# Kernel optimization log

Hardware: AMD Instinct MI355X
Metric: run time of the kernel (lower is better)

## Reference

```python
import jax, jax.numpy as jnp
import numpy as np

N, E, B = 30000, 480000, 64
F_IN, HID, ED = 128, 64, 32
NEG, EPS = 0.2, 1e-5


def _add_self_loops(edge_index, edge_attr):
    # PyG add_self_loops with fill_value='mean': self-loop edge_attr of node i
    # is the mean of edge_attr over edges whose destination is i.
    src, dst = edge_index[0], edge_index[1]
    cnt = jax.ops.segment_sum(jnp.ones((edge_attr.shape[0],), edge_attr.dtype), dst, num_segments=N)
    mean = jax.ops.segment_sum(edge_attr, dst, num_segments=N) / jnp.maximum(cnt, 1.0)[:, None]
    loop = jnp.arange(N)
    return jnp.concatenate([src, loop]), jnp.concatenate([dst, loop]), jnp.concatenate([edge_attr, mean], axis=0)


def _gat_conv(x, src, dst, ea, W, We, a_s, a_d, a_e, bias, H, Fo):
    xs = (x @ W).reshape(-1, H, Fo)              # [N, H, Fo]
    al_src = (xs * a_s).sum(-1)                  # [N, H]
    al_dst = (xs * a_d).sum(-1)                  # [N, H]
    ef = (ea @ We).reshape(-1, H, Fo)            # [Et, H, Fo]
    alpha = al_src[src] + al_dst[dst] + (ef * a_e).sum(-1)   # [Et, H]
    alpha = jax.nn.leaky_relu(alpha, NEG)
    # softmax over incoming edges of each destination node (segment softmax)
    m = jax.ops.segment_max(alpha, dst, num_segments=N)
    ex = jnp.exp(alpha - m[dst])
    s = jax.ops.segment_sum(ex, dst, num_segments=N)
    w = ex / s[dst]                              # [Et, H]
    out = jax.ops.segment_sum(xs[src] * w[:, :, None], dst, num_segments=N)
    return out.reshape(-1, H * Fo) + bias


def _bn(x, g, b):
    # BatchNorm1d in training mode: biased batch statistics over nodes
    mu = x.mean(0)
    var = x.var(0)
    return (x - mu) * jax.lax.rsqrt(var + EPS) * g + b


def _pool(x, batch, Wg, bg):
    # GlobalAttention: softmax(gate_nn(x)) per graph, weighted sum of x
    gate = (x @ Wg + bg)[:, 0]                   # [N]
    m = jax.ops.segment_max(gate, batch, num_segments=B)
    e = jnp.exp(gate - m[batch])
    s = jax.ops.segment_sum(e, batch, num_segments=B)
    w = e / s[batch]
    return jax.ops.segment_sum(x * w[:, None], batch, num_segments=B)   # [B, HID]


def setup_inputs():
    k = jax.random.split(jax.random.key(0), 16)
    g = lambda i, shape, fan: jax.random.normal(k[i], shape, jnp.float32) / np.sqrt(fan)
    return {
        "x": jax.random.normal(k[0], (N, F_IN), jnp.float32),
        "edge_attr": jax.random.normal(k[1], (E, ED), jnp.float32),
        "edge_index": jax.random.randint(k[2], (2, E), 0, N),
        "batch": jnp.sort(jax.random.randint(k[3], (N,), 0, B)),
        "W1": g(4, (F_IN, 4 * HID), F_IN),
        "We1": g(5, (ED, 4 * HID), ED),
        "att_src1": g(6, (4, HID), HID),
        "att_dst1": g(7, (4, HID), HID),
        "att_edge1": g(8, (4, HID), HID),
        "bias1": jnp.zeros((4 * HID,), jnp.float32),
        "g1": jnp.ones((4 * HID,), jnp.float32),
        "b1": jnp.zeros((4 * HID,), jnp.float32),
        "W2": g(9, (4 * HID, HID), 4 * HID),
        "We2": g(10, (ED, HID), ED),
        "att_src2": g(11, (1, HID), HID),
        "att_dst2": g(12, (1, HID), HID),
        "att_edge2": g(13, (1, HID), HID),
        "bias2": jnp.zeros((HID,), jnp.float32),
        "g2": jnp.ones((HID,), jnp.float32),
        "b2": jnp.zeros((HID,), jnp.float32),
        "Wg": g(14, (HID, 1), HID),
        "bg": jnp.zeros((1,), jnp.float32),
    }


def reference(x, edge_attr, edge_index, batch, W1, We1, att_src1, att_dst1, att_edge1, bias1, g1, b1, W2, We2, att_src2, att_dst2, att_edge2, bias2, g2, b2, Wg, bg):
    src, dst, ea = _add_self_loops(edge_index, edge_attr)
    h = jax.nn.relu(_bn(_gat_conv(x, src, dst, ea, W1, We1, att_src1, att_dst1, att_edge1, bias1, 4, HID), g1, b1))
    h = jax.nn.relu(_bn(_gat_conv(h, src, dst, ea, W2, We2, att_src2, att_dst2, att_edge2, bias2, 1, HID), g2, b2))
    return _pool(h, batch, Wg, bg)
```

## Files before the change

### kernel.cpp

```cpp
#include <hip/hip_runtime.h>
#include <math.h>

#define NN 30000
#define EE 480000
#define BB 64

typedef __bf16 b16x8 __attribute__((ext_vector_type(8)));
typedef float  f32x4 __attribute__((ext_vector_type(4)));
typedef unsigned short u16x8 __attribute__((ext_vector_type(8)));

__device__ __forceinline__ float wsum64(float v){
  #pragma unroll
  for (int m = 32; m >= 1; m >>= 1) v += __shfl_xor(v, m, 64);
  return v;
}
__device__ __forceinline__ float wmax64(float v){
  #pragma unroll
  for (int m = 32; m >= 1; m >>= 1) v = fmaxf(v, __shfl_xor(v, m, 64));
  return v;
}
__device__ __forceinline__ float wsum16(float v){
  #pragma unroll
  for (int m = 1; m < 16; m <<= 1) v += __shfl_xor(v, m, 64);
  return v;
}
__device__ __forceinline__ unsigned short f2b(float f){
  union { float f; unsigned u; } v; v.f = f;
  unsigned r = v.u + 0x7fffu + ((v.u >> 16) & 1u);
  return (unsigned short)(r >> 16);
}
__device__ __forceinline__ float b2f(unsigned short u){
  union { unsigned u; float f; } v; v.u = ((unsigned)u) << 16;
  return v.f;
}

__global__ void hist_kernel(const int* __restrict__ dst, int* __restrict__ deg){
  int e = blockIdx.x*256 + threadIdx.x;
  if (e < EE) atomicAdd(&deg[dst[e]], 1);
}

__global__ __launch_bounds__(256) void scan_kernel(const int* __restrict__ deg, int* __restrict__ rowptr){
  __shared__ int s[256];
  __shared__ int wred[4];
  const int b = blockIdx.x, tid = threadIdx.x;
  const int base = b*256;
  int part = 0;
  for (int idx = tid; idx < base; idx += 256) part += deg[idx];
  #pragma unroll
  for (int m = 32; m >= 1; m >>= 1) part += __shfl_xor(part, m, 64);
  if ((tid & 63) == 0) wred[tid >> 6] = part;
  __syncthreads();
  int offset = wred[0] + wred[1] + wred[2] + wred[3];
  int n = base + tid;
  int d = (n < NN) ? deg[n] : 0;
  s[tid] = d;
  __syncthreads();
  for (int off = 1; off < 256; off <<= 1){
    int v = (tid >= off) ? s[tid - off] : 0;
    __syncthreads();
    s[tid] += v;
    __syncthreads();
  }
  if (n < NN) rowptr[n] = offset + s[tid] - d;
  if (b == 0 && tid == 0) rowptr[NN] = EE;
}

__global__ void prep_kernel(const float* __restrict__ W1, const float* __restrict__ W2,
                            const float* __restrict__ We1, const float* __restrict__ ae1,
                            const float* __restrict__ We2, const float* __restrict__ ae2,
                            unsigned short* __restrict__ W1t, unsigned short* __restrict__ W2t,
                            float* __restrict__ wae){
  int t = threadIdx.x, b = blockIdx.x;
  if (b < 128){
    W1t[t*128 + b] = f2b(W1[b*256 + t]);
  } else if (b < 384){
    int k = b - 128;
    if (t < 64) W2t[t*256 + k] = f2b(W2[k*64 + t]);
  } else {
    if (t < 128){
      int h = t >> 5, k = t & 31;
      float s = 0.f;
      for (int f = 0; f < 64; f++) s += We1[k*256 + h*64 + f] * ae1[h*64 + f];
      wae[h*32 + k] = s;
    } else if (t < 160){
      int k = t - 128;
      float s = 0.f;
      for (int f = 0; f < 64; f++) s += We2[k*64 + f] * ae2[f];
      wae[128 + k] = s;
    }
  }
}

__global__ __launch_bounds__(256) void edot_scatter_kernel(const float* __restrict__ ea,
    const float* __restrict__ wae, const int* __restrict__ src, const int* __restrict__ dst,
    const int* __restrict__ rowptr, int* __restrict__ cursor, float* __restrict__ rec){
  __shared__ float s_w[160];
  if (threadIdx.x < 160) s_w[threadIdx.x] = wae[threadIdx.x];
  __syncthreads();
  const int lane = threadIdx.x & 63;
  const int il = lane & 7;
  const int e = blockIdx.x*32 + (threadIdx.x >> 3);
  if (e >= EE) return;
  float4 v = *(const float4*)(ea + (size_t)e*32 + il*4);
  float dots[5];
  #pragma unroll
  for (int h = 0; h < 5; h++){
    float4 w = *(const float4*)&s_w[h*32 + il*4];
    dots[h] = v.x*w.x + v.y*w.y + v.z*w.z + v.w*w.w;
  }
  #pragma unroll
  for (int m = 1; m < 8; m <<= 1)
    #pragma unroll
    for (int h = 0; h < 5; h++) dots[h] += __shfl_xor(dots[h], m, 64);
  int slot = 0;
  if (il == 0){
    int dd = dst[e];
    slot = rowptr[dd] + atomicAdd(&cursor[dd], 1);
  }
  slot = __shfl(slot, lane & ~7, 64);
  if (il == 0){
    float4 lo; lo.x = dots[0]; lo.y = dots[1]; lo.z = dots[2]; lo.w = dots[3];
    *(float4*)(rec + (size_t)slot*8) = lo;
  } else if (il == 1){
    float4 hi; hi.x = dots[4]; hi.y = __int_as_float(src[e]); hi.z = 0.f; hi.w = 0.f;
    *(float4*)(rec + (size_t)slot*8 + 4) = hi;
  }
}

__global__ __launch_bounds__(256) void gemm1_mfma(const float* __restrict__ x,
    const unsigned short* __restrict__ Bt, const float* __restrict__ a_s, const float* __restrict__ a_d,
    unsigned short* __restrict__ out, float* __restrict__ alsrc, float* __restrict__ aldst){
  __shared__ unsigned short As[128*136];
  __shared__ unsigned short Bs[64*136];
  const int tid = threadIdx.x;
  const int w = tid >> 6, lane = tid & 63;
  const int c = lane & 15, gq = lane >> 4;
  const int m0 = blockIdx.x * 128;
  #pragma unroll
  for (int q = 0; q < 16; q++){
    int ch = tid*16 + q;
    int r = ch >> 5, off = (ch & 31)*4;
    int grow = m0 + r;
    ushort4 o;
    if (grow < NN){
      float4 v = *(const float4*)(x + (size_t)grow*128 + off);
      o.x = f2b(v.x); o.y = f2b(v.y); o.z = f2b(v.z); o.w = f2b(v.w);
    } else o = make_ushort4(0,0,0,0);
    *(ushort4*)&As[r*136 + off] = o;
  }
  #pragma unroll
  for (int q = 0; q < 4; q++){
    int ch = tid*4 + q;
    int n = ch >> 4, off = (ch & 15)*8;
    *(ulonglong2*)&Bs[n*136 + off] = *(const ulonglong2*)(Bt + (size_t)n*128 + off);
  }
  __syncthreads();
  for (int head = 0; head < 4; head++){
    f32x4 acc[2][4];
    #pragma unroll
    for (int mt = 0; mt < 2; mt++)
      #pragma unroll
      for (int nt = 0; nt < 4; nt++) acc[mt][nt] = (f32x4){0.f,0.f,0.f,0.f};
    #pragma unroll
    for (int k0 = 0; k0 < 128; k0 += 32){
      b16x8 afr[2], bfr[4];
      #pragma unroll
      for (int mt = 0; mt < 2; mt++)
        afr[mt] = *(const b16x8*)&As[(w*32 + mt*16 + c)*136 + k0 + gq*8];
      #pragma unroll
      for (int nt = 0; nt < 4; nt++)
        bfr[nt] = *(const b16x8*)&Bs[(nt*16 + c)*136 + k0 + gq*8];
      #pragma unroll
      for (int mt = 0; mt < 2; mt++)
        #pragma unroll
        for (int nt = 0; nt < 4; nt++)
          acc[mt][nt] = __builtin_amdgcn_mfma_f32_16x16x32_bf16(afr[mt], bfr[nt], acc[mt][nt], 0, 0, 0);
    }
    __syncthreads();
    if (head < 3){
      #pragma unroll
      for (int q = 0; q < 4; q++){
        int ch = tid*4 + q;
        int n = ch >> 4, off = (ch & 15)*8;
        *(ulonglong2*)&Bs[n*136 + off] = *(const ulonglong2*)(Bt + (size_t)((head+1)*64 + n)*128 + off);
      }
    }
    float asv[4], adv[4];
    #pragma unroll
    for (int nt = 0; nt < 4; nt++){
      asv[nt] = a_s[head*64 + nt*16 + c];
      adv[nt] = a_d[head*64 + nt*16 + c];
    }
    #pragma unroll
    for (int mt = 0; mt < 2; mt++){
      int base_row = m0 + w*32 + mt*16 + gq*4;
      #pragma unroll
      for (int r = 0; r < 4; r++){
        int row = base_row + r;
        float ps = 0.f, pd = 0.f;
        #pragma unroll
        for (int nt = 0; nt < 4; nt++){
          ps += acc[mt][nt][r] * asv[nt];
          pd += acc[mt][nt][r] * adv[nt];
        }
        ps = wsum16(ps); pd = wsum16(pd);
        if (row < NN){
          if (c == 0){
            alsrc[(size_t)row*4 + head] = ps;
            aldst[(size_t)row*4 + head] = pd;
          }
          #pragma unroll
          for (int nt = 0; nt < 4; nt++)
            out[(size_t)row*256 + head*64 + nt*16 + c] = f2b(acc[mt][nt][r]);
        }
      }
    }
    if (head < 3) __syncthreads();
  }
}

__global__ __launch_bounds__(256) void gemm2_mfma(const unsigned short* __restrict__ Ab,
    const unsigned short* __restrict__ Bt,
    const float* __restrict__ cs, const float* __restrict__ csq,
    const float* __restrict__ g, const float* __restrict__ b,
    const float* __restrict__ a_s, const float* __restrict__ a_d,
    unsigned short* __restrict__ out, float* __restrict__ alsrc, float* __restrict__ aldst){
  __shared__ unsigned short As[128*136];
  __shared__ unsigned short Bs[64*136];
  __shared__ float s_scale[256], s_shift[256];
  const int tid = threadIdx.x;
  const int w = tid >> 6, lane = tid & 63;
  const int c = lane & 15, gq = lane >> 4;
  const int m0 = blockIdx.x * 128;
  if (tid < 256){
    float mu  = cs[tid]  * (1.f/NN);
    float var = csq[tid] * (1.f/NN) - mu*mu;
    float rs  = rsqrtf(var + 1e-5f);
    float sc  = rs * g[tid];
    s_scale[tid] = sc;
    s_shift[tid] = b[tid] - mu*sc;
  }
  __syncthreads();
  f32x4 acc[2][4];
  #pragma unroll
  for (int mt = 0; mt < 2; mt++)
    #pragma unroll
    for (int nt = 0; nt < 4; nt++) acc[mt][nt] = (f32x4){0.f,0.f,0.f,0.f};
  for (int kp = 0; kp < 256; kp += 128){
    #pragma unroll
    for (int q = 0; q < 16; q++){
      int ch = tid*16 + q;
      int r = ch >> 5, off = (ch & 31)*4;
      int grow = m0 + r;
      ushort4 o;
      if (grow < NN){
        ushort4 v = *(const ushort4*)(Ab + (size_t)grow*256 + kp + off);
        float4 sc = *(const float4*)&s_scale[kp + off];
        float4 sh = *(const float4*)&s_shift[kp + off];
        o.x = f2b(fmaxf(fmaf(b2f(v.x), sc.x, sh.x), 0.f));
        o.y = f2b(fmaxf(fmaf(b2f(v.y), sc.y, sh.y), 0.f));
        o.z = f2b(fmaxf(fmaf(b2f(v.z), sc.z, sh.z), 0.f));
        o.w = f2b(fmaxf(fmaf(b2f(v.w), sc.w, sh.w), 0.f));
      } else o = make_ushort4(0,0,0,0);
      *(ushort4*)&As[r*136 + off] = o;
    }
    #pragma unroll
    for (int q = 0; q < 4; q++){
      int ch = tid*4 + q;
      int n = ch >> 4, off = (ch & 15)*8;
      *(ulonglong2*)&Bs[n*136 + off] = *(const ulonglong2*)(Bt + (size_t)n*256 + kp + off);
    }
    __syncthreads();
    #pragma unroll
    for (int k0 = 0; k0 < 128; k0 += 32){
      b16x8 afr[2], bfr[4];
      #pragma unroll
      for (int mt = 0; mt < 2; mt++)
        afr[mt] = *(const b16x8*)&As[(w*32 + mt*16 + c)*136 + k0 + gq*8];
      #pragma unroll
      for (int nt = 0; nt < 4; nt++)
        bfr[nt] = *(const b16x8*)&Bs[(nt*16 + c)*136 + k0 + gq*8];
      #pragma unroll
      for (int mt = 0; mt < 2; mt++)
        #pragma unroll
        for (int nt = 0; nt < 4; nt++)
          acc[mt][nt] = __builtin_amdgcn_mfma_f32_16x16x32_bf16(afr[mt], bfr[nt], acc[mt][nt], 0, 0, 0);
    }
    __syncthreads();
  }
  float asv[4], adv[4];
  #pragma unroll
  for (int nt = 0; nt < 4; nt++){
    asv[nt] = a_s[nt*16 + c];
    adv[nt] = a_d[nt*16 + c];
  }
  #pragma unroll
  for (int mt = 0; mt < 2; mt++){
    int base_row = m0 + w*32 + mt*16 + gq*4;
    #pragma unroll
    for (int r = 0; r < 4; r++){
      int row = base_row + r;
      float ps = 0.f, pd = 0.f;
      #pragma unroll
      for (int nt = 0; nt < 4; nt++){
        ps += acc[mt][nt][r] * asv[nt];
        pd += acc[mt][nt][r] * adv[nt];
      }
      ps = wsum16(ps); pd = wsum16(pd);
      if (row < NN){
        if (c == 0){
          alsrc[row] = ps;
          aldst[row] = pd;
        }
        #pragma unroll
        for (int nt = 0; nt < 4; nt++)
          out[(size_t)row*64 + nt*16 + c] = f2b(acc[mt][nt][r]);
      }
    }
  }
}

template<int H>
__global__ __launch_bounds__(256) void agg_kernel(const int* __restrict__ rowptr,
    const float* __restrict__ rec,
    const float* __restrict__ al_src, const float* __restrict__ al_dst,
    const unsigned short* __restrict__ xsb, const float* __restrict__ bias,
    unsigned short* __restrict__ outb, float* __restrict__ outf){
  constexpr int CH = 128;
  __shared__ float s_e_all[4][CH*H];
  __shared__ int   s_src_all[4][CH];
  const int wid  = threadIdx.x >> 6;
  const int lane = threadIdx.x & 63;
  const int i = blockIdx.x*4 + wid;
  float* s_e  = s_e_all[wid];
  int*   s_src = s_src_all[wid];
  const int r0 = rowptr[i];
  const int d  = rowptr[i+1] - r0;
  float ad[H], asi[H];
  #pragma unroll
  for (int h = 0; h < H; h++){ ad[h] = al_dst[(size_t)i*H+h]; asi[h] = al_src[(size_t)i*H+h]; }
  float sesum[H], m[H];
  #pragma unroll
  for (int h = 0; h < H; h++){ sesum[h] = 0.f; m[h] = -1e30f; }
  for (int t = lane; t < d; t += 64){
    const float* rp = rec + (size_t)(r0 + t)*8;
    float al[H];
    int sn;
    if constexpr (H == 4){
      float4 ev = *(const float4*)rp;
      float2 hi = *(const float2*)(rp + 4);
      sn = __float_as_int(hi.y);
      float4 av = *(const float4*)(al_src + (size_t)sn*4);
      al[0]=av.x+ad[0]+ev.x; al[1]=av.y+ad[1]+ev.y; al[2]=av.z+ad[2]+ev.z; al[3]=av.w+ad[3]+ev.w;
      sesum[0]+=ev.x; sesum[1]+=ev.y; sesum[2]+=ev.z; sesum[3]+=ev.w;
    } else {
      float2 hi = *(const float2*)(rp + 4);
      sn = __float_as_int(hi.y);
      al[0] = al_src[sn] + ad[0] + hi.x;
      sesum[0] += hi.x;
    }
    if (t < CH) s_src[t] = sn;
    #pragma unroll
    for (int h = 0; h < H; h++){
      float a = al[h]; a = a > 0.f ? a : 0.2f*a;
      if (t < CH) s_e[t*H+h] = a;
      m[h] = fmaxf(m[h], a);
    }
  }
  float invd = (d > 0) ? 1.f/(float)d : 0.f;
  float sa[H];
  #pragma unroll
  for (int h = 0; h < H; h++){
    sesum[h] = wsum64(sesum[h]);
    m[h] = wmax64(m[h]);
    float a = asi[h] + ad[h] + sesum[h]*invd;
    sa[h] = a > 0.f ? a : 0.2f*a;
    m[h] = fmaxf(m[h], sa[h]);
  }
  float acc8[8];
  #pragma unroll
  for (int j = 0; j < 8; j++) acc8[j] = 0.f;
  float dpart[H];
  #pragma unroll
  for (int h = 0; h < H; h++) dpart[h] = 0.f;
  const int half = lane >> 5, il5 = lane & 31;
  const int grp  = lane >> 3, il3 = lane & 7;
  int c0 = 0;
  while (c0 < d){
    int cl = min(CH, d - c0);
    if (c0 > 0){
      for (int t = lane; t < cl; t += 64){
        const float* rp = rec + (size_t)(r0 + c0 + t)*8;
        if constexpr (H == 4){
          float4 ev = *(const float4*)rp;
          float2 hi = *(const float2*)(rp + 4);
          int sn = __float_as_int(hi.y);
          s_src[t] = sn;
          float4 av = *(const float4*)(al_src + (size_t)sn*4);
          float a0=av.x+ad[0]+ev.x, a1=av.y+ad[1]+ev.y, a2=av.z+ad[2]+ev.z, a3=av.w+ad[3]+ev.w;
          s_e[t*4+0]=a0>0.f?a0:0.2f*a0; s_e[t*4+1]=a1>0.f?a1:0.2f*a1;
          s_e[t*4+2]=a2>0.f?a2:0.2f*a2; s_e[t*4+3]=a3>0.f?a3:0.2f*a3;
        } else {
          float2 hi = *(const float2*)(rp + 4);
          int sn = __float_as_int(hi.y);
          s_src[t] = sn;
          float a = al_src[sn] + ad[0] + hi.x;
          s_e[t] = a > 0.f ? a : 0.2f*a;
        }
      }
    }
    for (int t = lane; t < cl; t += 64){
      #pragma unroll
      for (int h = 0; h < H; h++){
        float e = __expf(s_e[t*H+h] - m[h]);
        s_e[t*H+h] = e;
        dpart[h] += e;
      }
    }
    __builtin_amdgcn_wave_barrier();
    if constexpr (H == 4){
      const int hd = il5 >> 3;
      for (int t = half; t < cl; t += 2){
        int sn = s_src[t];
        float wv = s_e[t*4 + hd];
        u16x8 u = *(const u16x8*)(xsb + (size_t)sn*256 + il5*8);
        #pragma unroll
        for (int j = 0; j < 8; j++) acc8[j] += wv * b2f(u[j]);
      }
    } else {
      for (int t = grp; t < cl; t += 8){
        int sn = s_src[t];
        float wv = s_e[t];
        u16x8 u = *(const u16x8*)(xsb + (size_t)sn*64 + il3*8);
        #pragma unroll
        for (int j = 0; j < 8; j++) acc8[j] += wv * b2f(u[j]);
      }
    }
    __builtin_amdgcn_wave_barrier();
    c0 += CH;
  }
  float es[H];
  #pragma unroll
  for (int h = 0; h < H; h++) es[h] = __expf(sa[h] - m[h]);
  if (lane == 0){
    #pragma unroll
    for (int h = 0; h < H; h++) dpart[h] += es[h];
  }
  if constexpr (H == 4){
    if (half == 0){
      float wv = es[il5 >> 3];
      u16x8 u = *(const u16x8*)(xsb + (size_t)i*256 + il5*8);
      #pragma unroll
      for (int j = 0; j < 8; j++) acc8[j] += wv * b2f(u[j]);
    }
  } else {
    if (grp == 0){
      float wv = es[0];
      u16x8 u = *(const u16x8*)(xsb + (size_t)i*64 + il3*8);
      #pragma unroll
      for (int j = 0; j < 8; j++) acc8[j] += wv * b2f(u[j]);
    }
  }
  float denom[H];
  #pragma unroll
  for (int h = 0; h < H; h++) denom[h] = wsum64(dpart[h]);
  if constexpr (H == 4){
    #pragma unroll
    for (int j = 0; j < 8; j++) acc8[j] += __shfl_xor(acc8[j], 32, 64);
    if (lane < 32){
      float inv = 1.f / denom[il5 >> 3];
      u16x8 o;
      #pragma unroll
      for (int j = 0; j < 8; j++) o[j] = f2b(acc8[j]*inv + bias[il5*8 + j]);
      *(u16x8*)(outb + (size_t)i*256 + il5*8) = o;
    }
  } else {
    #pragma unroll
    for (int j = 0; j < 8; j++){
      acc8[j] += __shfl_xor(acc8[j], 8, 64);
      acc8[j] += __shfl_xor(acc8[j], 16, 64);
      acc8[j] += __shfl_xor(acc8[j], 32, 64);
    }
    if (lane < 8){
      float inv = 1.f / denom[0];
      float4 o0, o1;
      o0.x = acc8[0]*inv + bias[il3*8+0]; o0.y = acc8[1]*inv + bias[il3*8+1];
      o0.z = acc8[2]*inv + bias[il3*8+2]; o0.w = acc8[3]*inv + bias[il3*8+3];
      o1.x = acc8[4]*inv + bias[il3*8+4]; o1.y = acc8[5]*inv + bias[il3*8+5];
      o1.z = acc8[6]*inv + bias[il3*8+6]; o1.w = acc8[7]*inv + bias[il3*8+7];
      *(float4*)(outf + (size_t)i*64 + il3*8)     = o0;
      *(float4*)(outf + (size_t)i*64 + il3*8 + 4) = o1;
    }
  }
}

__global__ __launch_bounds__(256) void bn_stats_b16_kernel(const unsigned short* __restrict__ h,
    float* __restrict__ cs, float* __restrict__ csq){
  __shared__ float s_red[4][256], q_red[4][256];
  const int tid = threadIdx.x;
  const int wv = tid >> 6, lane = tid & 63;
  const int rg = lane >> 5, cg = lane & 31;
  float s8[8], q8[8];
  #pragma unroll
  for (int j = 0; j < 8; j++){ s8[j] = 0.f; q8[j] = 0.f; }
  for (int chunk = blockIdx.x; chunk < 3750; chunk += 256){
    int r = chunk*8 + wv*2 + rg;
    u16x8 u = *(const u16x8*)(h + (size_t)r*256 + cg*8);
    #pragma unroll
    for (int j = 0; j < 8; j++){
      float v = b2f(u[j]);
      s8[j] += v; q8[j] += v*v;
    }
  }
  #pragma unroll
  for (int j = 0; j < 8; j++){
    s8[j] += __shfl_xor(s8[j], 32, 64);
    q8[j] += __shfl_xor(q8[j], 32, 64);
  }
  if (lane < 32){
    #pragma unroll
    for (int j = 0; j < 8; j++){
      s_red[wv][cg*8 + j] = s8[j];
      q_red[wv][cg*8 + j] = q8[j];
    }
  }
  __syncthreads();
  if (tid < 256){
    float ts = s_red[0][tid] + s_red[1][tid] + s_red[2][tid] + s_red[3][tid];
    float tq = q_red[0][tid] + q_red[1][tid] + q_red[2][tid] + q_red[3][tid];
    atomicAdd(&cs[tid], ts);
    atomicAdd(&csq[tid], tq);
  }
}

__global__ __launch_bounds__(256) void bn_stats_f32_kernel(const float* __restrict__ h,
    float* __restrict__ cs, float* __restrict__ csq){
  int col = threadIdx.x & 63;
  int ro  = threadIdx.x >> 6;
  float s = 0.f, s2 = 0.f;
  for (int r = blockIdx.x*4 + ro; r < NN; r += 1024){
    float v = h[(size_t)r*64 + col];
    s += v; s2 += v*v;
  }
  atomicAdd(&cs[col], s);
  atomicAdd(&csq[col], s2);
}

__global__ __launch_bounds__(256) void gate_kernel(const float* __restrict__ h,
    const float* __restrict__ cs, const float* __restrict__ csq,
    const float* __restrict__ g2, const float* __restrict__ b2,
    const float* __restrict__ Wg, const float* __restrict__ bg,
    float* __restrict__ hn, float* __restrict__ gate){
  int wid = threadIdx.x >> 6, lane = threadIdx.x & 63;
  int n = blockIdx.x*4 + wid;
  float mu  = cs[lane]  * (1.f/NN);
  float var = csq[lane] * (1.f/NN) - mu*mu;
  float rs  = rsqrtf(var + 1e-5f);
  float sc  = rs * g2[lane];
  float sh  = b2[lane] - mu*sc;
  float v = h[(size_t)n*64 + lane];
  float xx = fmaxf(fmaf(v, sc, sh), 0.f);
  hn[(size_t)n*64 + lane] = xx;
  float p = wsum64(xx * Wg[lane]);
  if (lane == 0) gate[n] = p + bg[0];
}

__global__ __launch_bounds__(256) void pool_kernel(const int* __restrict__ batch,
    const float* __restrict__ gate, const float* __restrict__ hn, float* __restrict__ out){
  __shared__ float red[256];
  __shared__ float a_red[4][64], w_red[4];
  __shared__ int seb[2];
  int b = blockIdx.x, tid = threadIdx.x;
  int wv = tid >> 6, lane = tid & 63;
  if (tid < 2){
    int target = b + tid;
    int lo = 0, hi = NN;
    while (lo < hi){ int mid = (lo+hi) >> 1; if (batch[mid] < target) lo = mid+1; else hi = mid; }
    seb[tid] = lo;
  }
  __syncthreads();
  int s = seb[0], e = seb[1];
  if (e <= s){ if (tid < 64) out[b*64 + tid] = 0.f; return; }
  float mloc = -1e30f;
  for (int n = s + tid; n < e; n += 256) mloc = fmaxf(mloc, gate[n]);
  mloc = wmax64(mloc);
  if (lane == 0) red[wv] = mloc;
  __syncthreads();
  float m = fmaxf(fmaxf(red[0], red[1]), fmaxf(red[2], red[3]));
  int rgrp = tid >> 4, cq = tid & 15;
  f32x4 acc = (f32x4){0.f,0.f,0.f,0.f};
  float wp = 0.f;
  for (int n = s + rgrp; n < e; n += 16){
    float wgt = __expf(gate[n] - m);
    float4 v = *(const float4*)(hn + (size_t)n*64 + cq*4);
    acc[0] += wgt*v.x; acc[1] += wgt*v.y; acc[2] += wgt*v.z; acc[3] += wgt*v.w;
    if (cq == 0) wp += wgt;
  }
  #pragma unroll
  for (int j = 0; j < 4; j++){
    acc[j] += __shfl_xor(acc[j], 16, 64);
    acc[j] += __shfl_xor(acc[j], 32, 64);
  }
  wp += __shfl_xor(wp, 16, 64);
  wp += __shfl_xor(wp, 32, 64);
  if (lane < 16){
    #pragma unroll
    for (int j = 0; j < 4; j++) a_red[wv][lane*4 + j] = acc[j];
  }
  if (lane == 0) w_red[wv] = wp;
  __syncthreads();
  if (tid < 64){
    float tot = a_red[0][tid] + a_red[1][tid] + a_red[2][tid] + a_red[3][tid];
    float wsm = w_red[0] + w_red[1] + w_red[2] + w_red[3];
    out[b*64 + tid] = tot / wsm;
  }
}

extern "C" void kernel_launch(void* const* d_in, const int* in_sizes, int n_in,
                              void* d_out, int out_size, void* d_ws, size_t ws_size,
                              hipStream_t stream){
  const float* x     = (const float*)d_in[0];
  const float* ea    = (const float*)d_in[1];
  const int*   ei    = (const int*)d_in[2];
  const int*   batch = (const int*)d_in[3];
  const float* W1    = (const float*)d_in[4];
  const float* We1   = (const float*)d_in[5];
  const float* as1   = (const float*)d_in[6];
  const float* ad1   = (const float*)d_in[7];
  const float* ae1   = (const float*)d_in[8];
  const float* bias1 = (const float*)d_in[9];
  const float* g1    = (const float*)d_in[10];
  const float* b1    = (const float*)d_in[11];
  const float* W2    = (const float*)d_in[12];
  const float* We2   = (const float*)d_in[13];
  const float* as2   = (const float*)d_in[14];
  const float* ad2   = (const float*)d_in[15];
  const float* ae2   = (const float*)d_in[16];
  const float* bias2 = (const float*)d_in[17];
  const float* g2    = (const float*)d_in[18];
  const float* b2    = (const float*)d_in[19];
  const float* Wg    = (const float*)d_in[20];
  const float* bg    = (const float*)d_in[21];
  const int* srcI = ei;
  const int* dstI = ei + EE;

  char* ws = (char*)d_ws;
  int*   deg    = (int*)(ws + 0);
  int*   cursor = (int*)(ws + 120064);
  float* stats  = (float*)(ws + 240128);
  int*   rowptr = (int*)(ws + 244224);
  float* wae    = (float*)(ws + 364288);
  unsigned short* W1t = (unsigned short*)(ws + 365056);
  unsigned short* W2t = (unsigned short*)(ws + 430592);
  float* alsrc  = (float*)(ws + 463360);
  float* aldst  = (float*)(ws + 943360);
  float* gateb  = (float*)(ws + 1423360);
  float* rec    = (float*)(ws + 1543424);
  unsigned short* xs1b = (unsigned short*)(ws + 16903424);
  unsigned short* h1b  = (unsigned short*)(ws + 32263424);
  unsigned short* xs2b = (unsigned short*)(ws + 47623424);
  float* h2     = (float*)(ws + 51463424);
  float* hn     = (float*)(ws + 59143424);

  (void)hipMemsetAsync(ws, 0, 244224, stream);

  hist_kernel<<<1875, 256, 0, stream>>>(dstI, deg);
  scan_kernel<<<118, 256, 0, stream>>>(deg, rowptr);
  prep_kernel<<<385, 256, 0, stream>>>(W1, W2, We1, ae1, We2, ae2, W1t, W2t, wae);
  edot_scatter_kernel<<<15000, 256, 0, stream>>>(ea, wae, srcI, dstI, rowptr, cursor, rec);

  gemm1_mfma<<<235, 256, 0, stream>>>(x, W1t, as1, ad1, xs1b, alsrc, aldst);
  agg_kernel<4><<<7500, 256, 0, stream>>>(rowptr, rec, alsrc, aldst, xs1b, bias1, h1b, nullptr);
  bn_stats_b16_kernel<<<256, 256, 0, stream>>>(h1b, stats + 0, stats + 256);

  gemm2_mfma<<<235, 256, 0, stream>>>(h1b, W2t, stats + 0, stats + 256, g1, b1,
                                      as2, ad2, xs2b, alsrc, aldst);
  agg_kernel<1><<<7500, 256, 0, stream>>>(rowptr, rec, alsrc, aldst, xs2b, bias2, nullptr, h2);
  bn_stats_f32_kernel<<<256, 256, 0, stream>>>(h2, stats + 512, stats + 576);

  gate_kernel<<<7500, 256, 0, stream>>>(h2, stats + 512, stats + 576, g2, b2, Wg, bg, hn, gateb);
  pool_kernel<<<64, 256, 0, stream>>>(batch, gateb, hn, (float*)d_out);
}
```

Baseline: 364.4 us.

## Split edge-dot and CSR scatter into separate kernels; unroll aggregation gathers

The fused edge-dot/scatter kernel becomes two kernels. One computes the per-edge attention dot products into dense arrays, and a second does the atomic slot assignment and writes the CSR records with one thread per edge. Separately, the aggregation loops for both heads are unrolled by four and by two, so several independent gathered row loads are in flight before their weighted accumulation. The split adds an extra kernel launch and an intermediate round trip through memory, in exchange for coalesced dot computation and less divergent atomic work.

```diff
diff --git a/kernel.cpp b/kernel.cpp
--- a/kernel.cpp
+++ b/kernel.cpp
@@ -91,9 +91,8 @@
   }
 }
 
-__global__ __launch_bounds__(256) void edot_scatter_kernel(const float* __restrict__ ea,
-    const float* __restrict__ wae, const int* __restrict__ src, const int* __restrict__ dst,
-    const int* __restrict__ rowptr, int* __restrict__ cursor, float* __restrict__ rec){
+__global__ __launch_bounds__(256) void edot_kernel(const float* __restrict__ ea,
+    const float* __restrict__ wae, float4* __restrict__ dlo, float2* __restrict__ dhi){
   __shared__ float s_w[160];
   if (threadIdx.x < 160) s_w[threadIdx.x] = wae[threadIdx.x];
   __syncthreads();
@@ -112,19 +111,27 @@
   for (int m = 1; m < 8; m <<= 1)
     #pragma unroll
     for (int h = 0; h < 5; h++) dots[h] += __shfl_xor(dots[h], m, 64);
-  int slot = 0;
-  if (il == 0){
-    int dd = dst[e];
-    slot = rowptr[dd] + atomicAdd(&cursor[dd], 1);
-  }
-  slot = __shfl(slot, lane & ~7, 64);
   if (il == 0){
     float4 lo; lo.x = dots[0]; lo.y = dots[1]; lo.z = dots[2]; lo.w = dots[3];
-    *(float4*)(rec + (size_t)slot*8) = lo;
+    dlo[e] = lo;
   } else if (il == 1){
-    float4 hi; hi.x = dots[4]; hi.y = __int_as_float(src[e]); hi.z = 0.f; hi.w = 0.f;
-    *(float4*)(rec + (size_t)slot*8 + 4) = hi;
-  }
+    float2 hi; hi.x = dots[4]; hi.y = 0.f;
+    dhi[e] = hi;
+  }
+}
+
+__global__ __launch_bounds__(256) void scatter_kernel(const float4* __restrict__ dlo,
+    const float2* __restrict__ dhi, const int* __restrict__ src, const int* __restrict__ dst,
+    const int* __restrict__ rowptr, int* __restrict__ cursor, float* __restrict__ rec){
+  int e = blockIdx.x*256 + threadIdx.x;
+  if (e >= EE) return;
+  int dd = dst[e];
+  int slot = rowptr[dd] + atomicAdd(&cursor[dd], 1);
+  float4 lo = dlo[e];
+  float2 hi = dhi[e];
+  float4 hiv; hiv.x = hi.x; hiv.y = __int_as_float(src[e]); hiv.z = 0.f; hiv.w = 0.f;
+  *(float4*)(rec + (size_t)slot*8) = lo;
+  *(float4*)(rec + (size_t)slot*8 + 4) = hiv;
 }
 
 __global__ __launch_bounds__(256) void gemm1_mfma(const float* __restrict__ x,
@@ -420,7 +427,22 @@
     __builtin_amdgcn_wave_barrier();
     if constexpr (H == 4){
       const int hd = il5 >> 3;
-      for (int t = half; t < cl; t += 2){
+      int t = half;
+      for (; t + 6 < cl; t += 8){
+        int sn0 = s_src[t],   sn1 = s_src[t+2], sn2 = s_src[t+4], sn3 = s_src[t+6];
+        float w0 = s_e[t*4+hd],     w1 = s_e[(t+2)*4+hd];
+        float w2 = s_e[(t+4)*4+hd], w3 = s_e[(t+6)*4+hd];
+        u16x8 u0 = *(const u16x8*)(xsb + (size_t)sn0*256 + il5*8);
+        u16x8 u1 = *(const u16x8*)(xsb + (size_t)sn1*256 + il5*8);
+        u16x8 u2 = *(const u16x8*)(xsb + (size_t)sn2*256 + il5*8);
+        u16x8 u3 = *(const u16x8*)(xsb + (size_t)sn3*256 + il5*8);
+        #pragma unroll
+        for (int j = 0; j < 8; j++){
+          acc8[j] += w0*b2f(u0[j]); acc8[j] += w1*b2f(u1[j]);
+          acc8[j] += w2*b2f(u2[j]); acc8[j] += w3*b2f(u3[j]);
+        }
+      }
+      for (; t < cl; t += 2){
         int sn = s_src[t];
         float wv = s_e[t*4 + hd];
         u16x8 u = *(const u16x8*)(xsb + (size_t)sn*256 + il5*8);
@@ -428,7 +450,18 @@
         for (int j = 0; j < 8; j++) acc8[j] += wv * b2f(u[j]);
       }
     } else {
-      for (int t = grp; t < cl; t += 8){
+      int t = grp;
+      for (; t + 8 < cl; t += 16){
+        int sn0 = s_src[t], sn1 = s_src[t+8];
+        float w0 = s_e[t], w1 = s_e[t+8];
+        u16x8 u0 = *(const u16x8*)(xsb + (size_t)sn0*64 + il3*8);
+        u16x8 u1 = *(const u16x8*)(xsb + (size_t)sn1*64 + il3*8);
+        #pragma unroll
+        for (int j = 0; j < 8; j++){
+          acc8[j] += w0*b2f(u0[j]); acc8[j] += w1*b2f(u1[j]);
+        }
+      }
+      for (; t < cl; t += 8){
         int sn = s_src[t];
         float wv = s_e[t];
         u16x8 u = *(const u16x8*)(xsb + (size_t)sn*64 + il3*8);
@@ -661,13 +694,16 @@
   unsigned short* xs2b = (unsigned short*)(ws + 47623424);
   float* h2     = (float*)(ws + 51463424);
   float* hn     = (float*)(ws + 59143424);
+  float4* dlo   = (float4*)(ws + 66823424);
+  float2* dhi   = (float2*)(ws + 74503424);
 
   (void)hipMemsetAsync(ws, 0, 244224, stream);
 
   hist_kernel<<<1875, 256, 0, stream>>>(dstI, deg);
   scan_kernel<<<118, 256, 0, stream>>>(deg, rowptr);
   prep_kernel<<<385, 256, 0, stream>>>(W1, W2, We1, ae1, We2, ae2, W1t, W2t, wae);
-  edot_scatter_kernel<<<15000, 256, 0, stream>>>(ea, wae, srcI, dstI, rowptr, cursor, rec);
+  edot_kernel<<<15000, 256, 0, stream>>>(ea, wae, dlo, dhi);
+  scatter_kernel<<<1875, 256, 0, stream>>>(dlo, dhi, srcI, dstI, rowptr, cursor, rec);
 
   gemm1_mfma<<<235, 256, 0, stream>>>(x, W1t, as1, ad1, xs1b, alsrc, aldst);
   agg_kernel<4><<<7500, 256, 0, stream>>>(rowptr, rec, alsrc, aldst, xs1b, bias1, h1b, nullptr);
```

Result: slower. 382.4 us (+4.9%).

## Split GEMM work across more blocks and use one thread per edge

Applied to the files above, without the earlier changes.

gemm1 now launches one block per (row tile, head) instead of looping over the four heads inside a block, which gives four times as many blocks. gemm2 drops to 64-row tiles so twice as many blocks launch. The edge dot/scatter kernel now uses one thread per edge with sequential float4 loads instead of eight lanes per edge with shuffles. The aim is to fill more CUs and cut shuffle overhead. The cost is that each gemm1 block reloads and reconverts the x tile four times, and per-thread edge loads become strided and less coalesced.

```diff
diff --git a/kernel.cpp b/kernel.cpp
--- a/kernel.cpp
+++ b/kernel.cpp
@@ -91,40 +91,29 @@
   }
 }
 
-__global__ __launch_bounds__(256) void edot_scatter_kernel(const float* __restrict__ ea,
+__global__ __launch_bounds__(256) void edge_kernel(const float* __restrict__ ea,
     const float* __restrict__ wae, const int* __restrict__ src, const int* __restrict__ dst,
     const int* __restrict__ rowptr, int* __restrict__ cursor, float* __restrict__ rec){
-  __shared__ float s_w[160];
-  if (threadIdx.x < 160) s_w[threadIdx.x] = wae[threadIdx.x];
-  __syncthreads();
-  const int lane = threadIdx.x & 63;
-  const int il = lane & 7;
-  const int e = blockIdx.x*32 + (threadIdx.x >> 3);
+  int e = blockIdx.x*256 + threadIdx.x;
   if (e >= EE) return;
-  float4 v = *(const float4*)(ea + (size_t)e*32 + il*4);
-  float dots[5];
-  #pragma unroll
-  for (int h = 0; h < 5; h++){
-    float4 w = *(const float4*)&s_w[h*32 + il*4];
-    dots[h] = v.x*w.x + v.y*w.y + v.z*w.z + v.w*w.w;
-  }
-  #pragma unroll
-  for (int m = 1; m < 8; m <<= 1)
-    #pragma unroll
-    for (int h = 0; h < 5; h++) dots[h] += __shfl_xor(dots[h], m, 64);
-  int slot = 0;
-  if (il == 0){
-    int dd = dst[e];
-    slot = rowptr[dd] + atomicAdd(&cursor[dd], 1);
-  }
-  slot = __shfl(slot, lane & ~7, 64);
-  if (il == 0){
-    float4 lo; lo.x = dots[0]; lo.y = dots[1]; lo.z = dots[2]; lo.w = dots[3];
-    *(float4*)(rec + (size_t)slot*8) = lo;
-  } else if (il == 1){
-    float4 hi; hi.x = dots[4]; hi.y = __int_as_float(src[e]); hi.z = 0.f; hi.w = 0.f;
-    *(float4*)(rec + (size_t)slot*8 + 4) = hi;
-  }
+  int dd = dst[e];
+  int slot = rowptr[dd] + atomicAdd(&cursor[dd], 1);
+  int sv = src[e];
+  const float4* row = (const float4*)(ea + (size_t)e*32);
+  float dots[5] = {0.f, 0.f, 0.f, 0.f, 0.f};
+  #pragma unroll
+  for (int q = 0; q < 8; q++){
+    float4 v = row[q];
+    #pragma unroll
+    for (int h = 0; h < 5; h++){
+      float4 w = *(const float4*)(wae + h*32 + q*4);
+      dots[h] += v.x*w.x + v.y*w.y + v.z*w.z + v.w*w.w;
+    }
+  }
+  float4 lo; lo.x = dots[0]; lo.y = dots[1]; lo.z = dots[2]; lo.w = dots[3];
+  float4 hi; hi.x = dots[4]; hi.y = __int_as_float(sv); hi.z = 0.f; hi.w = 0.f;
+  *(float4*)(rec + (size_t)slot*8) = lo;
+  *(float4*)(rec + (size_t)slot*8 + 4) = hi;
 }
 
 __global__ __launch_bounds__(256) void gemm1_mfma(const float* __restrict__ x,
@@ -136,6 +125,7 @@
   const int w = tid >> 6, lane = tid & 63;
   const int c = lane & 15, gq = lane >> 4;
   const int m0 = blockIdx.x * 128;
+  const int head = blockIdx.y;
   #pragma unroll
   for (int q = 0; q < 16; q++){
     int ch = tid*16 + q;
@@ -152,70 +142,58 @@
   for (int q = 0; q < 4; q++){
     int ch = tid*4 + q;
     int n = ch >> 4, off = (ch & 15)*8;
-    *(ulonglong2*)&Bs[n*136 + off] = *(const ulonglong2*)(Bt + (size_t)n*128 + off);
-  }
-  __syncthreads();
-  for (int head = 0; head < 4; head++){
-    f32x4 acc[2][4];
+    *(ulonglong2*)&Bs[n*136 + off] = *(const ulonglong2*)(Bt + (size_t)(head*64 + n)*128 + off);
+  }
+  __syncthreads();
+  f32x4 acc[2][4];
+  #pragma unroll
+  for (int mt = 0; mt < 2; mt++)
+    #pragma unroll
+    for (int nt = 0; nt < 4; nt++) acc[mt][nt] = (f32x4){0.f,0.f,0.f,0.f};
+  #pragma unroll
+  for (int k0 = 0; k0 < 128; k0 += 32){
+    b16x8 afr[2], bfr[4];
     #pragma unroll
     for (int mt = 0; mt < 2; mt++)
-      #pragma unroll
-      for (int nt = 0; nt < 4; nt++) acc[mt][nt] = (f32x4){0.f,0.f,0.f,0.f};
-    #pragma unroll
-    for (int k0 = 0; k0 < 128; k0 += 32){
-      b16x8 afr[2], bfr[4];
-      #pragma unroll
-      for (int mt = 0; mt < 2; mt++)
-        afr[mt] = *(const b16x8*)&As[(w*32 + mt*16 + c)*136 + k0 + gq*8];
+      afr[mt] = *(const b16x8*)&As[(w*32 + mt*16 + c)*136 + k0 + gq*8];
+    #pragma unroll
+    for (int nt = 0; nt < 4; nt++)
+      bfr[nt] = *(const b16x8*)&Bs[(nt*16 + c)*136 + k0 + gq*8];
+    #pragma unroll
+    for (int mt = 0; mt < 2; mt++)
       #pragma unroll
       for (int nt = 0; nt < 4; nt++)
-        bfr[nt] = *(const b16x8*)&Bs[(nt*16 + c)*136 + k0 + gq*8];
-      #pragma unroll
-      for (int mt = 0; mt < 2; mt++)
+        acc[mt][nt] = __builtin_amdgcn_mfma_f32_16x16x32_bf16(afr[mt], bfr[nt], acc[mt][nt], 0, 0, 0);
+  }
+  float asv[4], adv[4];
+  #pragma unroll
+  for (int nt = 0; nt < 4; nt++){
+    asv[nt] = a_s[head*64 + nt*16 + c];
+    adv[nt] = a_d[head*64 + nt*16 + c];
+  }
+  #pragma unroll
+  for (int mt = 0; mt < 2; mt++){
+    int base_row = m0 + w*32 + mt*16 + gq*4;
+    #pragma unroll
+    for (int r = 0; r < 4; r++){
+      int row = base_row + r;
+      float ps = 0.f, pd = 0.f;
+      #pragma unroll
+      for (int nt = 0; nt < 4; nt++){
+        ps += acc[mt][nt][r] * asv[nt];
+        pd += acc[mt][nt][r] * adv[nt];
+      }
+      ps = wsum16(ps); pd = wsum16(pd);
+      if (row < NN){
+        if (c == 0){
+          alsrc[(size_t)row*4 + head] = ps;
+          aldst[(size_t)row*4 + head] = pd;
+        }
         #pragma unroll
         for (int nt = 0; nt < 4; nt++)
-          acc[mt][nt] = __builtin_amdgcn_mfma_f32_16x16x32_bf16(afr[mt], bfr[nt], acc[mt][nt], 0, 0, 0);
-    }
-    __syncthreads();
-    if (head < 3){
-      #pragma unroll
-      for (int q = 0; q < 4; q++){
-        int ch = tid*4 + q;
-        int n = ch >> 4, off = (ch & 15)*8;
-        *(ulonglong2*)&Bs[n*136 + off] = *(const ulonglong2*)(Bt + (size_t)((head+1)*64 + n)*128 + off);
+          out[(size_t)row*256 + head*64 + nt*16 + c] = f2b(acc[mt][nt][r]);
       }
     }
-    float asv[4], adv[4];
-    #pragma unroll
-    for (int nt = 0; nt < 4; nt++){
-      asv[nt] = a_s[head*64 + nt*16 + c];
-      adv[nt] = a_d[head*64 + nt*16 + c];
-    }
-    #pragma unroll
-    for (int mt = 0; mt < 2; mt++){
-      int base_row = m0 + w*32 + mt*16 + gq*4;
-      #pragma unroll
-      for (int r = 0; r < 4; r++){
-        int row = base_row + r;
-        float ps = 0.f, pd = 0.f;
-        #pragma unroll
-        for (int nt = 0; nt < 4; nt++){
-          ps += acc[mt][nt][r] * asv[nt];
-          pd += acc[mt][nt][r] * adv[nt];
-        }
-        ps = wsum16(ps); pd = wsum16(pd);
-        if (row < NN){
-          if (c == 0){
-            alsrc[(size_t)row*4 + head] = ps;
-            aldst[(size_t)row*4 + head] = pd;
-          }
-          #pragma unroll
-          for (int nt = 0; nt < 4; nt++)
-            out[(size_t)row*256 + head*64 + nt*16 + c] = f2b(acc[mt][nt][r]);
-        }
-      }
-    }
-    if (head < 3) __syncthreads();
   }
 }
 
@@ -225,14 +203,14 @@
     const float* __restrict__ g, const float* __restrict__ b,
     const float* __restrict__ a_s, const float* __restrict__ a_d,
     unsigned short* __restrict__ out, float* __restrict__ alsrc, float* __restrict__ aldst){
-  __shared__ unsigned short As[128*136];
+  __shared__ unsigned short As[64*136];
   __shared__ unsigned short Bs[64*136];
   __shared__ float s_scale[256], s_shift[256];
   const int tid = threadIdx.x;
   const int w = tid >> 6, lane = tid & 63;
   const int c = lane & 15, gq = lane >> 4;
-  const int m0 = blockIdx.x * 128;
-  if (tid < 256){
+  const int m0 = blockIdx.x * 64;
+  {
     float mu  = cs[tid]  * (1.f/NN);
     float var = csq[tid] * (1.f/NN) - mu*mu;
     float rs  = rsqrtf(var + 1e-5f);
@@ -241,15 +219,13 @@
     s_shift[tid] = b[tid] - mu*sc;
   }
   __syncthreads();
-  f32x4 acc[2][4];
-  #pragma unroll
-  for (int mt = 0; mt < 2; mt++)
-    #pragma unroll
-    for (int nt = 0; nt < 4; nt++) acc[mt][nt] = (f32x4){0.f,0.f,0.f,0.f};
+  f32x4 acc[4];
+  #pragma unroll
+  for (int nt = 0; nt < 4; nt++) acc[nt] = (f32x4){0.f,0.f,0.f,0.f};
   for (int kp = 0; kp < 256; kp += 128){
     #pragma unroll
-    for (int q = 0; q < 16; q++){
-      int ch = tid*16 + q;
+    for (int q = 0; q < 8; q++){
+      int ch = tid*8 + q;
       int r = ch >> 5, off = (ch & 31)*4;
       int grow = m0 + r;
       ushort4 o;
@@ -273,18 +249,14 @@
     __syncthreads();
     #pragma unroll
     for (int k0 = 0; k0 < 128; k0 += 32){
-      b16x8 afr[2], bfr[4];
-      #pragma unroll
-      for (int mt = 0; mt < 2; mt++)
-        afr[mt] = *(const b16x8*)&As[(w*32 + mt*16 + c)*136 + k0 + gq*8];
+      b16x8 afr = *(const b16x8*)&As[(w*16 + c)*136 + k0 + gq*8];
+      b16x8 bfr[4];
       #pragma unroll
       for (int nt = 0; nt < 4; nt++)
         bfr[nt] = *(const b16x8*)&Bs[(nt*16 + c)*136 + k0 + gq*8];
       #pragma unroll
-      for (int mt = 0; mt < 2; mt++)
-        #pragma unroll
-        for (int nt = 0; nt < 4; nt++)
-          acc[mt][nt] = __builtin_amdgcn_mfma_f32_16x16x32_bf16(afr[mt], bfr[nt], acc[mt][nt], 0, 0, 0);
+      for (int nt = 0; nt < 4; nt++)
+        acc[nt] = __builtin_amdgcn_mfma_f32_16x16x32_bf16(afr, bfr[nt], acc[nt], 0, 0, 0);
     }
     __syncthreads();
   }
@@ -294,28 +266,25 @@
     asv[nt] = a_s[nt*16 + c];
     adv[nt] = a_d[nt*16 + c];
   }
-  #pragma unroll
-  for (int mt = 0; mt < 2; mt++){
-    int base_row = m0 + w*32 + mt*16 + gq*4;
-    #pragma unroll
-    for (int r = 0; r < 4; r++){
-      int row = base_row + r;
-      float ps = 0.f, pd = 0.f;
-      #pragma unroll
-      for (int nt = 0; nt < 4; nt++){
-        ps += acc[mt][nt][r] * asv[nt];
-        pd += acc[mt][nt][r] * adv[nt];
+  int base_row = m0 + w*16 + gq*4;
+  #pragma unroll
+  for (int r = 0; r < 4; r++){
+    int row = base_row + r;
+    float ps = 0.f, pd = 0.f;
+    #pragma unroll
+    for (int nt = 0; nt < 4; nt++){
+      ps += acc[nt][r] * asv[nt];
+      pd += acc[nt][r] * adv[nt];
+    }
+    ps = wsum16(ps); pd = wsum16(pd);
+    if (row < NN){
+      if (c == 0){
+        alsrc[row] = ps;
+        aldst[row] = pd;
       }
-      ps = wsum16(ps); pd = wsum16(pd);
-      if (row < NN){
-        if (c == 0){
-          alsrc[row] = ps;
-          aldst[row] = pd;
-        }
-        #pragma unroll
-        for (int nt = 0; nt < 4; nt++)
-          out[(size_t)row*64 + nt*16 + c] = f2b(acc[mt][nt][r]);
-      }
+      #pragma unroll
+      for (int nt = 0; nt < 4; nt++)
+        out[(size_t)row*64 + nt*16 + c] = f2b(acc[nt][r]);
     }
   }
 }
@@ -667,13 +636,13 @@
   hist_kernel<<<1875, 256, 0, stream>>>(dstI, deg);
   scan_kernel<<<118, 256, 0, stream>>>(deg, rowptr);
   prep_kernel<<<385, 256, 0, stream>>>(W1, W2, We1, ae1, We2, ae2, W1t, W2t, wae);
-  edot_scatter_kernel<<<15000, 256, 0, stream>>>(ea, wae, srcI, dstI, rowptr, cursor, rec);
-
-  gemm1_mfma<<<235, 256, 0, stream>>>(x, W1t, as1, ad1, xs1b, alsrc, aldst);
+  edge_kernel<<<1875, 256, 0, stream>>>(ea, wae, srcI, dstI, rowptr, cursor, rec);
+
+  gemm1_mfma<<<dim3(235, 4), 256, 0, stream>>>(x, W1t, as1, ad1, xs1b, alsrc, aldst);
   agg_kernel<4><<<7500, 256, 0, stream>>>(rowptr, rec, alsrc, aldst, xs1b, bias1, h1b, nullptr);
   bn_stats_b16_kernel<<<256, 256, 0, stream>>>(h1b, stats + 0, stats + 256);
 
-  gemm2_mfma<<<235, 256, 0, stream>>>(h1b, W2t, stats + 0, stats + 256, g1, b1,
+  gemm2_mfma<<<470, 256, 0, stream>>>(h1b, W2t, stats + 0, stats + 256, g1, b1,
                                       as2, ad2, xs2b, alsrc, aldst);
   agg_kernel<1><<<7500, 256, 0, stream>>>(rowptr, rec, alsrc, aldst, xs2b, bias2, nullptr, h2);
   bn_stats_f32_kernel<<<256, 256, 0, stream>>>(h2, stats + 512, stats + 576);
```

Result: slower. 380.2 us (+4.3%).
